# Kernel tuning notes

Hardware: AMD Instinct MI355X
Metric: run time of the kernel (lower is better)

Reference implementation:

```python
import jax, jax.numpy as jnp
import numpy as np

RES = 64      # resolution (D=H=W)
WIDTH = 32    # FNO channel width
MODES = 8     # retained Fourier modes per dim
NL = 4        # FNO layers
NU = 0.000185 # viscosity
FCH = 128     # projection hidden width
B = 4


def setup_inputs() -> dict:
    key = jax.random.key(0)
    ks = jax.random.split(key, 8)
    u = jax.random.normal(ks[0], (B, 3, RES, RES, RES), jnp.float32)
    s = 1.0 / (WIDTH * WIDTH)
    fc0_w = jax.random.normal(ks[1], (3, WIDTH), jnp.float32) * (1.0 / 3.0) ** 0.5
    fc0_b = jnp.zeros((WIDTH,), jnp.float32)
    # (layer, corner, in, out, m1, m2, m3, re/im)
    spec_w = jax.random.normal(ks[2], (NL, 4, WIDTH, WIDTH, MODES, MODES, MODES, 2), jnp.float32) * s
    w_pw = jax.random.normal(ks[3], (NL, WIDTH, WIDTH), jnp.float32) * (1.0 / WIDTH) ** 0.5
    b_pw = jnp.zeros((NL, WIDTH), jnp.float32)
    fc1_w = jax.random.normal(ks[4], (WIDTH, FCH), jnp.float32) * (1.0 / WIDTH) ** 0.5
    fc1_b = jnp.zeros((FCH,), jnp.float32)
    fc2_w = jax.random.normal(ks[5], (FCH, 6), jnp.float32) * (1.0 / FCH) ** 0.5
    fc2_b = jnp.zeros((6,), jnp.float32)
    return dict(u=u, fc0_w=fc0_w, fc0_b=fc0_b, spec_w=spec_w, w_pw=w_pw,
                b_pw=b_pw, fc1_w=fc1_w, fc1_b=fc1_b, fc2_w=fc2_w, fc2_b=fc2_b)


def _pointwise(x, w, b):
    # 1x1x1 conv: (B,C,D,H,W) x (C,O) -> (B,O,D,H,W)
    return jnp.einsum('bcdhw,co->bodhw', x, w) + b[None, :, None, None, None]


def _spectral_conv(x, wf):
    m = MODES
    Bn, C, D, H, W = x.shape
    ft = jnp.fft.rfftn(x, axes=(-3, -2, -1))           # (B,C,D,H,W//2+1) complex64
    w = wf[..., 0] + 1j * wf[..., 1]                   # (4,C,O,m,m,m)
    mul = lambda blk, ww: jnp.einsum('bixyz,ioxyz->boxyz', blk, ww)
    out = jnp.zeros((Bn, w.shape[2], D, H, W // 2 + 1), jnp.complex64)
    out = out.at[:, :, :m, :m, :m].set(mul(ft[:, :, :m, :m, :m], w[0]))
    out = out.at[:, :, -m:, :m, :m].set(mul(ft[:, :, -m:, :m, :m], w[1]))
    out = out.at[:, :, :m, -m:, :m].set(mul(ft[:, :, :m, -m:, :m], w[2]))
    out = out.at[:, :, -m:, -m:, :m].set(mul(ft[:, :, -m:, -m:, :m], w[3]))
    return jnp.fft.irfftn(out, s=(D, H, W), axes=(-3, -2, -1))


def _fno(u, fc0_w, fc0_b, spec_w, w_pw, b_pw, fc1_w, fc1_b, fc2_w, fc2_b):
    x = _pointwise(u, fc0_w, fc0_b)
    for l in range(NL):
        x1 = _spectral_conv(x, spec_w[l])
        x2 = _pointwise(x, w_pw[l], b_pw[l])
        x = x1 + x2
        if l < NL - 1:
            x = jax.nn.gelu(x)
    x = jax.nn.gelu(_pointwise(x, fc1_w, fc1_b))
    return _pointwise(x, fc2_w, fc2_b)


def _ns_hard_core(u):
    # du/dt = -(u.grad)u + nu * lap(u), periodic central differences
    dx = 2.0 * np.pi / RES
    conv = jnp.zeros_like(u)
    diff = jnp.zeros_like(u)
    for j in range(3):
        ax = 2 + j
        up = jnp.roll(u, -1, axis=ax)
        um = jnp.roll(u, 1, axis=ax)
        du = (up - um) / (2.0 * dx)          # d u_i / d x_j for all i
        conv = conv - u[:, j:j + 1] * du
        diff = diff + (up - 2.0 * u + um) / (dx * dx)
    return conv + NU * diff


def reference(u, fc0_w, fc0_b, spec_w, w_pw, b_pw, fc1_w, fc1_b, fc2_w, fc2_b):
    du_hard = _ns_hard_core(u)
    tau = _fno(u, fc0_w, fc0_b, spec_w, w_pw, b_pw, fc1_w, fc1_b, fc2_w, fc2_b)
    du_dt = du_hard + tau[:, :3] * 0.001
    return du_dt, tau
```

## Files before the change

### kernel.cpp

```cpp
#include <hip/hip_runtime.h>
#include <hip/hip_bf16.h>

#define RES 64
#define WIDTH 32
#define MODES 8
#define R3 262144
#define TWO_PI_OVER_64 0.09817477042468103f

__device__ __forceinline__ float geluf(float x) {
    float g = 1.5957691216057308f * (x + 0.044715f * x * x * x);
    return x * __builtin_amdgcn_rcpf(1.0f + __expf(-g));
}

constexpr double tcos_(double x) {
    double r = 1.0, term = 1.0;
    for (int i = 1; i <= 12; i++) { term *= -x * x / ((2.0 * i - 1.0) * (2.0 * i)); r += term; }
    return r;
}
constexpr double tsin_(double x) {
    double r = x, term = x;
    for (int i = 1; i <= 12; i++) { term *= -x * x / ((2.0 * i) * (2.0 * i + 1.0)); r += term; }
    return r;
}
struct Tw64 { float c[64]; float s[64]; };
constexpr Tw64 mkTw() {
    Tw64 t{};
    const double th = 6.283185307179586476925286766559 / 64.0;
    for (int i = 0; i < 64; i++) {
        double a = th * (i <= 32 ? i : i - 64);
        t.c[i] = (float)tcos_(a);
        t.s[i] = (float)tsin_(a);
    }
    return t;
}
constexpr Tw64 TWT = mkTw();

__global__ void k_fc0(const float* __restrict__ u, const float* __restrict__ w,
                      const float* __restrict__ bias, float* __restrict__ X) {
    __shared__ float ws[96];
    __shared__ float bs[32];
    int t = threadIdx.x;
    if (t < 96) ws[t] = w[t];
    if (t < 32) bs[t] = bias[t];
    __syncthreads();
    size_t s = (size_t)blockIdx.x * 256 + t;
    int b = (int)(s >> 18);
    size_t p = s & (R3 - 1);
    const float* ub = u + (size_t)b * 3 * R3;
    float u0 = ub[p], u1 = ub[R3 + p], u2 = ub[2 * R3 + p];
    float* xb = X + (size_t)b * 32 * R3;
    #pragma unroll
    for (int o = 0; o < 32; o++) {
        xb[(size_t)o * R3 + p] = bs[o] + u0 * ws[o] + u1 * ws[32 + o] + u2 * ws[64 + o];
    }
}

__global__ void __launch_bounds__(256, 6)
k_fwd_zy(const float* __restrict__ X, float2* __restrict__ S2) {
    int t = threadIdx.x;
    int q = t >> 6, y = t & 63;
    int bcx0 = blockIdx.x * 4;
    __shared__ float2 zt[4][8][66];
    __shared__ float2 tw[64];
    if (t < 64) { float s, c; __sincosf(TWO_PI_OVER_64 * t, &s, &c); tw[t] = make_float2(c, s); }

    const float* row = X + (size_t)(bcx0 + q) * 4096 + (size_t)y * 64;
    float re[8], im[8];
    #pragma unroll
    for (int k = 0; k < 8; k++) { re[k] = 0.f; im[k] = 0.f; }
    #pragma unroll
    for (int zb = 0; zb < 8; zb++) {
        float xa[4], xb4[4];
        *(float4*)xa  = *(const float4*)(row + zb * 4);
        *(float4*)xb4 = *(const float4*)(row + zb * 4 + 32);
        #pragma unroll
        for (int j = 0; j < 4; j++) {
            int z = zb * 4 + j;
            float sv = xa[j] + xb4[j];
            float dv = xa[j] - xb4[j];
            #pragma unroll
            for (int k = 0; k < 8; k++) {
                float v = (k & 1) ? dv : sv;
                re[k] += v * TWT.c[(k * z) & 63];
                im[k] -= v * TWT.s[(k * z) & 63];
            }
        }
    }
    #pragma unroll
    for (int k = 0; k < 8; k++) zt[q][k][y] = make_float2(re[k], im[k]);
    __syncthreads();

    int l = t & 63;
    int jy = l >> 2, kp = l & 3;
    int f = jy < 8 ? jy : 48 + jy;
    int k0 = kp * 2;
    float re0 = 0.f, im0 = 0.f, re1 = 0.f, im1 = 0.f;
    #pragma unroll 8
    for (int yy = 0; yy < 64; yy++) {
        float2 w = tw[(f * yy) & 63];
        float2 v0 = zt[q][k0][yy];
        float2 v1 = zt[q][k0 + 1][yy];
        re0 += v0.x * w.x + v0.y * w.y;
        im0 += v0.y * w.x - v0.x * w.y;
        re1 += v1.x * w.x + v1.y * w.y;
        im1 += v1.y * w.x - v1.x * w.y;
    }
    float2* dst = S2 + (size_t)(bcx0 + q) * 128 + jy * 8 + k0;
    dst[0] = make_float2(re0, im0);
    dst[1] = make_float2(re1, im1);
}

__global__ void k_fwd_x(const float2* __restrict__ S2, float2* __restrict__ S3) {
    int bc = blockIdx.x >> 3, kz = blockIdx.x & 7;
    int t = threadIdx.x;
    __shared__ float2 in[64 * 16];
    __shared__ float2 tw[64];
    if (t < 64) { float s, c; __sincosf(TWO_PI_OVER_64 * t, &s, &c); tw[t] = make_float2(c, s); }
    #pragma unroll
    for (int i = 0; i < 4; i++) {
        int e = t + 256 * i;
        in[e] = S2[((size_t)bc * 1024 + e) * 8 + kz];
    }
    __syncthreads();
    int jx = t >> 4, jy = t & 15;
    int f = jx < 8 ? jx : 48 + jx;
    float re = 0.f, im = 0.f;
    for (int x = 0; x < 64; x++) {
        float2 v = in[x * 16 + jy];
        float2 w = tw[(f * x) & 63];
        re += v.x * w.x + v.y * w.y;
        im += v.y * w.x - v.x * w.y;
    }
    S3[(size_t)bc * 2048 + (size_t)t * 8 + kz] = make_float2(re, im);
}

__global__ void k_specmul(const float2* __restrict__ S3, const float* __restrict__ spec_w,
                          float2* __restrict__ S4, int layer) {
    int mp = blockIdx.x;
    int t = threadIdx.x;
    int jxy = mp >> 2;
    int kz0 = (mp & 3) * 2;
    int jy = jxy & 15, jx = jxy >> 4;
    int corner = (jx >= 8 ? 1 : 0) + (jy >= 8 ? 2 : 0);
    int m1 = jx & 7, m2 = jy & 7;
    int mode0 = jxy * 8 + kz0;
    __shared__ float4 W4[1024];
    __shared__ float2 inb[2][128];
    const float* wbase = spec_w + (size_t)layer * 4194304 + (size_t)corner * 1048576
                       + m1 * 128 + m2 * 16 + kz0 * 2;
    #pragma unroll
    for (int j = 0; j < 8; j++) {
        int e = t + 128 * j;
        int i = e >> 5, o = e & 31;
        W4[e] = *(const float4*)(wbase + (size_t)i * 32768 + (size_t)o * 1024);
    }
    inb[0][t] = S3[(size_t)t * 2048 + mode0];
    inb[1][t] = S3[(size_t)t * 2048 + mode0 + 1];
    __syncthreads();
    int b = t >> 5, o = t & 31;
    float re0 = 0.f, im0 = 0.f, re1 = 0.f, im1 = 0.f;
    #pragma unroll 8
    for (int i = 0; i < 32; i++) {
        float2 a0 = inb[0][b * 32 + i];
        float2 a1 = inb[1][b * 32 + i];
        float4 w = W4[i * 32 + o];
        re0 += a0.x * w.x - a0.y * w.y;
        im0 += a0.x * w.y + a0.y * w.x;
        re1 += a1.x * w.z - a1.y * w.w;
        im1 += a1.x * w.w + a1.y * w.z;
    }
    S4[(size_t)(b * 32 + o) * 2048 + mode0]     = make_float2(re0, im0);
    S4[(size_t)(b * 32 + o) * 2048 + mode0 + 1] = make_float2(re1, im1);
}

__global__ void k_inv_x(const float2* __restrict__ S4, float2* __restrict__ S5) {
    int bo = blockIdx.x >> 3, kz = blockIdx.x & 7;
    int t = threadIdx.x;
    __shared__ float2 in[256];
    __shared__ float2 tw[64];
    if (t < 64) { float s, c; __sincosf(TWO_PI_OVER_64 * t, &s, &c); tw[t] = make_float2(c, s); }
    in[t] = S4[(size_t)bo * 2048 + (size_t)t * 8 + kz];
    __syncthreads();
    int x = t & 63, g = t >> 6;
    #pragma unroll
    for (int m = 0; m < 4; m++) {
        int jy = g + 4 * m;
        float re = 0.f, im = 0.f;
        #pragma unroll
        for (int jx = 0; jx < 16; jx++) {
            int f = jx < 8 ? jx : 48 + jx;
            float2 v = in[jx * 16 + jy];
            float2 w = tw[(f * x) & 63];
            re += v.x * w.x - v.y * w.y;
            im += v.x * w.y + v.y * w.x;
        }
        S5[((size_t)bo * 64 + x) * 128 + jy * 8 + kz] = make_float2(re, im);
    }
}

__global__ void __launch_bounds__(256, 3)
k_inv_yz_pw(const float2* __restrict__ S5, const float* __restrict__ w_pw,
            const float* __restrict__ b_pw, float* __restrict__ X,
            int layer, int do_gelu) {
    int blk = blockIdx.x;
    int yg = blk & 3, x = (blk >> 2) & 63, b = blk >> 8;
    int t = threadIdx.x;
    __shared__ float2 s5s[32 * 132];
    __shared__ float2 st[256];
    __shared__ float xt[2048];
    __shared__ float2 tw[64];
    if (t < 64) { float s, c; __sincosf(TWO_PI_OVER_64 * t, &s, &c); tw[t] = make_float2(c, s); }
    #pragma unroll
    for (int i = 0; i < 8; i++) {
        int f4 = t + 256 * i;
        int o = f4 >> 6, j4 = f4 & 63;
        float4 v = ((const float4*)(S5 + ((size_t)(b * 32 + o) * 64 + x) * 128))[j4];
        *(float4*)(&s5s[o * 132 + j4 * 2]) = v;
    }
    __syncthreads();
    int z = t & 63, og = t >> 6;
    int og8 = og * 8;
    int og8u = __builtin_amdgcn_readfirstlane(og8);
    const float* wl = w_pw + layer * 1024 + og8u;
    const float* bl = b_pw + layer * 32 + og8u;
    float bt0 = bl[0], bt1 = bl[1], bt2 = bl[2], bt3 = bl[3];
    float bt4 = bl[4], bt5 = bl[5], bt6 = bl[6], bt7 = bl[7];
    float2 tz1 = tw[z];
    float2 tz2 = tw[(2 * z) & 63];
    float2 tz3 = tw[(3 * z) & 63];
    float2 tz4 = tw[(4 * z) & 63];
    float2 tz5 = tw[(5 * z) & 63];
    float2 tz6 = tw[(6 * z) & 63];
    float2 tz7 = tw[(7 * z) & 63];
    const float inv_n = 1.0f / 262144.0f;
    for (int yi = 0; yi < 16; yi++) {
        int y = yg * 16 + yi;
        {
            int o = t >> 3, k = t & 7;
            float re = 0.f, im = 0.f;
            #pragma unroll
            for (int jy = 0; jy < 16; jy++) {
                int f = jy < 8 ? jy : 48 + jy;
                float2 v = s5s[o * 132 + jy * 8 + k];
                float2 w = tw[(f * y) & 63];
                re += v.x * w.x - v.y * w.y;
                im += v.x * w.y + v.y * w.x;
            }
            st[t] = make_float2(re, im);
        }
        size_t base = (size_t)b * 8388608 + (size_t)(x * 64 + y) * 64;
        #pragma unroll
        for (int i = 0; i < 8; i++) {
            int e = t + 256 * i;
            int c = e >> 6, zz = e & 63;
            xt[e] = X[base + (size_t)c * R3 + zz];
        }
        __syncthreads();
#define INVZ_S(o) (st[(o) * 8 + 0].x \
        + 2.f * (st[(o) * 8 + 1].x * tz1.x - st[(o) * 8 + 1].y * tz1.y) \
        + 2.f * (st[(o) * 8 + 2].x * tz2.x - st[(o) * 8 + 2].y * tz2.y) \
        + 2.f * (st[(o) * 8 + 3].x * tz3.x - st[(o) * 8 + 3].y * tz3.y) \
        + 2.f * (st[(o) * 8 + 4].x * tz4.x - st[(o) * 8 + 4].y * tz4.y) \
        + 2.f * (st[(o) * 8 + 5].x * tz5.x - st[(o) * 8 + 5].y * tz5.y) \
        + 2.f * (st[(o) * 8 + 6].x * tz6.x - st[(o) * 8 + 6].y * tz6.y) \
        + 2.f * (st[(o) * 8 + 7].x * tz7.x - st[(o) * 8 + 7].y * tz7.y))
        float acc0 = bt0 + INVZ_S(og8 + 0) * inv_n;
        float acc1 = bt1 + INVZ_S(og8 + 1) * inv_n;
        float acc2 = bt2 + INVZ_S(og8 + 2) * inv_n;
        float acc3 = bt3 + INVZ_S(og8 + 3) * inv_n;
        float acc4 = bt4 + INVZ_S(og8 + 4) * inv_n;
        float acc5 = bt5 + INVZ_S(og8 + 5) * inv_n;
        float acc6 = bt6 + INVZ_S(og8 + 6) * inv_n;
        float acc7 = bt7 + INVZ_S(og8 + 7) * inv_n;
#undef INVZ_S
        #pragma unroll 4
        for (int c = 0; c < 32; c++) {
            float xc = xt[c * 64 + z];
            const float* wr = wl + c * 32;
            float w0 = wr[0], w1 = wr[1], w2 = wr[2], w3 = wr[3];
            float w4 = wr[4], w5 = wr[5], w6 = wr[6], w7 = wr[7];
            acc0 += xc * w0; acc1 += xc * w1; acc2 += xc * w2; acc3 += xc * w3;
            acc4 += xc * w4; acc5 += xc * w5; acc6 += xc * w6; acc7 += xc * w7;
        }
        __syncthreads();
        float r;
        r = do_gelu ? geluf(acc0) : acc0; X[base + (size_t)(og8 + 0) * R3 + z] = r;
        r = do_gelu ? geluf(acc1) : acc1; X[base + (size_t)(og8 + 1) * R3 + z] = r;
        r = do_gelu ? geluf(acc2) : acc2; X[base + (size_t)(og8 + 2) * R3 + z] = r;
        r = do_gelu ? geluf(acc3) : acc3; X[base + (size_t)(og8 + 3) * R3 + z] = r;
        r = do_gelu ? geluf(acc4) : acc4; X[base + (size_t)(og8 + 4) * R3 + z] = r;
        r = do_gelu ? geluf(acc5) : acc5; X[base + (size_t)(og8 + 5) * R3 + z] = r;
        r = do_gelu ? geluf(acc6) : acc6; X[base + (size_t)(og8 + 6) * R3 + z] = r;
        r = do_gelu ? geluf(acc7) : acc7; X[base + (size_t)(og8 + 7) * R3 + z] = r;
    }
}

typedef short bf16x8_t __attribute__((ext_vector_type(8)));
typedef float f32x4_t __attribute__((ext_vector_type(4)));

__device__ __forceinline__ float dpp_add16(float v) {
    int i;
    i = __builtin_amdgcn_update_dpp(0, __builtin_bit_cast(int, v), 0xB1, 0xF, 0xF, true);
    v += __builtin_bit_cast(float, i);
    i = __builtin_amdgcn_update_dpp(0, __builtin_bit_cast(int, v), 0x4E, 0xF, 0xF, true);
    v += __builtin_bit_cast(float, i);
    i = __builtin_amdgcn_update_dpp(0, __builtin_bit_cast(int, v), 0x141, 0xF, 0xF, true);
    v += __builtin_bit_cast(float, i);
    i = __builtin_amdgcn_update_dpp(0, __builtin_bit_cast(int, v), 0x140, 0xF, 0xF, true);
    v += __builtin_bit_cast(float, i);
    return v;
}

__global__ void __launch_bounds__(256, 2)
k_head(const float* __restrict__ X, const float* __restrict__ w1,
       const float* __restrict__ b1, const float* __restrict__ w2,
       const float* __restrict__ b2, float* __restrict__ tau_out) {
    int t = threadIdx.x;
    int lane = t & 63;
    int wv = t >> 6;
    int m = lane & 15;
    int g = lane >> 4;
    size_t sblock = (size_t)blockIdx.x * 256;
    int b = (int)(sblock >> 18);
    size_t pblock = sblock & (R3 - 1);
    const float* xb = X + (size_t)b * 8388608 + pblock;

    bf16x8_t Bhi[8], Blo[8];
    #pragma unroll
    for (int tt = 0; tt < 8; tt++) {
        #pragma unroll
        for (int j = 0; j < 8; j++) {
            float w = w1[(g * 8 + j) * 128 + tt * 16 + m];
            unsigned bits = __builtin_bit_cast(unsigned, w);
            float hf = __builtin_bit_cast(float, bits & 0xFFFF0000u);
            float lof = w - hf;
            unsigned lb = __builtin_bit_cast(unsigned, lof);
            Bhi[tt][j] = (short)(bits >> 16);
            Blo[tt][j] = (short)(lb >> 16);
        }
    }
    float w2r[8][6];
    #pragma unroll
    for (int tt = 0; tt < 8; tt++)
        #pragma unroll
        for (int o = 0; o < 6; o++) w2r[tt][o] = w2[(tt * 16 + m) * 6 + o];
    float b1r[8];
    #pragma unroll
    for (int tt = 0; tt < 8; tt++) b1r[tt] = b1[tt * 16 + m];
    float b2m = b2[m < 6 ? m : 0];

    for (int it = 0; it < 4; it++) {
        int s16 = wv * 64 + it * 16;
        bf16x8_t Ahi, Alo;
        #pragma unroll
        for (int j = 0; j < 8; j++) {
            float xv = xb[(size_t)(g * 8 + j) * R3 + s16 + m];
            unsigned bits = __builtin_bit_cast(unsigned, xv);
            float hf = __builtin_bit_cast(float, bits & 0xFFFF0000u);
            float lof = xv - hf;
            unsigned lb = __builtin_bit_cast(unsigned, lof);
            Ahi[j] = (short)(bits >> 16);
            Alo[j] = (short)(lb >> 16);
        }
        float p0[6] = {0.f, 0.f, 0.f, 0.f, 0.f, 0.f};
        float p1[6] = {0.f, 0.f, 0.f, 0.f, 0.f, 0.f};
        float p2[6] = {0.f, 0.f, 0.f, 0.f, 0.f, 0.f};
        float p3[6] = {0.f, 0.f, 0.f, 0.f, 0.f, 0.f};
        #pragma unroll
        for (int tt = 0; tt < 8; tt++) {
            f32x4_t d = {0.f, 0.f, 0.f, 0.f};
            d = __builtin_amdgcn_mfma_f32_16x16x32_bf16(Ahi, Bhi[tt], d, 0, 0, 0);
            d = __builtin_amdgcn_mfma_f32_16x16x32_bf16(Ahi, Blo[tt], d, 0, 0, 0);
            d = __builtin_amdgcn_mfma_f32_16x16x32_bf16(Alo, Bhi[tt], d, 0, 0, 0);
            float a0 = geluf(d[0] + b1r[tt]);
            float a1 = geluf(d[1] + b1r[tt]);
            float a2 = geluf(d[2] + b1r[tt]);
            float a3 = geluf(d[3] + b1r[tt]);
            #pragma unroll
            for (int o = 0; o < 6; o++) {
                float w = w2r[tt][o];
                p0[o] += a0 * w; p1[o] += a1 * w; p2[o] += a2 * w; p3[o] += a3 * w;
            }
        }
        float q0 = 0.f, q1 = 0.f, q2 = 0.f, q3 = 0.f;
        #pragma unroll
        for (int o = 0; o < 6; o++) {
            float r0 = dpp_add16(p0[o]);
            float r1 = dpp_add16(p1[o]);
            float r2 = dpp_add16(p2[o]);
            float r3 = dpp_add16(p3[o]);
            q0 = (m == o) ? r0 : q0;
            q1 = (m == o) ? r1 : q1;
            q2 = (m == o) ? r2 : q2;
            q3 = (m == o) ? r3 : q3;
        }
        if (m < 6) {
            float4 vv = make_float4(q0 + b2m, q1 + b2m, q2 + b2m, q3 + b2m);
            *(float4*)(tau_out + (size_t)b * 6 * R3 + (size_t)m * R3 + pblock + s16 + g * 4) = vv;
        }
    }
}

__global__ void k_hard(const float* __restrict__ u, const float* __restrict__ tau,
                       float* __restrict__ out0) {
    size_t s = (size_t)blockIdx.x * 256 + threadIdx.x;
    int bi = (int)(s >> 18);
    int b = bi / 3, i = bi % 3;
    size_t p = s & (R3 - 1);
    int x = (int)(p >> 12), y = ((int)p >> 6) & 63, z = (int)p & 63;
    const float dx = TWO_PI_OVER_64;
    const float inv2dx = 1.0f / (2.0f * dx);
    const float invdx2 = 1.0f / (dx * dx);
    const float* ub = u + (size_t)b * 3 * R3;
    const float* ui = ub + (size_t)i * R3;
    int xp = (x + 1) & 63, xm = (x + 63) & 63;
    int yp = (y + 1) & 63, ym = (y + 63) & 63;
    int zp = (z + 1) & 63, zm = (z + 63) & 63;
    float c0 = ui[p];
    float upx = ui[((size_t)xp << 12) | (y << 6) | z], umx = ui[((size_t)xm << 12) | (y << 6) | z];
    float upy = ui[((size_t)x << 12) | (yp << 6) | z], umy = ui[((size_t)x << 12) | (ym << 6) | z];
    float upz = ui[((size_t)x << 12) | (y << 6) | zp], umz = ui[((size_t)x << 12) | (y << 6) | zm];
    float u0c = ub[p], u1c = ub[R3 + p], u2c = ub[2 * R3 + p];
    float conv = -(u0c * (upx - umx) + u1c * (upy - umy) + u2c * (upz - umz)) * inv2dx;
    float diff = (upx + umx + upy + umy + upz + umz - 6.0f * c0) * invdx2;
    float tauv = tau[(size_t)b * 6 * R3 + (size_t)i * R3 + p];
    out0[s] = conv + 0.000185f * diff + 0.001f * tauv;
}

extern "C" void kernel_launch(void* const* d_in, const int* in_sizes, int n_in,
                              void* d_out, int out_size, void* d_ws, size_t ws_size,
                              hipStream_t stream) {
    const float* u      = (const float*)d_in[0];
    const float* fc0_w  = (const float*)d_in[1];
    const float* fc0_b  = (const float*)d_in[2];
    const float* spec_w = (const float*)d_in[3];
    const float* w_pw   = (const float*)d_in[4];
    const float* b_pw   = (const float*)d_in[5];
    const float* fc1_w  = (const float*)d_in[6];
    const float* fc1_b  = (const float*)d_in[7];
    const float* fc2_w  = (const float*)d_in[8];
    const float* fc2_b  = (const float*)d_in[9];
    float* out = (float*)d_out;

    float* X = (float*)d_ws;

    float2* S2 = (float2*)(out);
    float2* S3 = (float2*)(out + 2097152);
    float2* S4 = (float2*)(out + 2621440);
    float2* S5 = (float2*)(out + 3145728);

    k_fc0<<<4096, 256, 0, stream>>>(u, fc0_w, fc0_b, X);

    for (int l = 0; l < 4; l++) {
        k_fwd_zy<<<2048, 256, 0, stream>>>(X, S2);
        k_fwd_x<<<1024, 256, 0, stream>>>(S2, S3);
        k_specmul<<<1024, 128, 0, stream>>>(S3, spec_w, S4, l);
        k_inv_x<<<1024, 256, 0, stream>>>(S4, S5);
        k_inv_yz_pw<<<1024, 256, 0, stream>>>(S5, w_pw, b_pw, X, l, (l < 3) ? 1 : 0);
    }

    float* tau_out = out + (size_t)4 * 3 * R3;
    k_head<<<4096, 256, 0, stream>>>(X, fc1_w, fc1_b, fc2_w, fc2_b, tau_out);
    k_hard<<<12288, 256, 0, stream>>>(u, tau_out, out);
}
```

Baseline: 1.123 ms.

## Keep spectral coefficients in registers and prefetch next X row in inverse yz kernel

The inverse y/z transform plus pointwise kernel no longer stages the per-x spectral slab in shared memory. Each thread now loads its 16 coefficients straight into registers, and the next y-row of X is prefetched into registers while the current row is being computed. Dropping the large shared buffer frees LDS, and launch bounds go from 3 to 4 blocks per CU to raise occupancy. The trade-off is more register pressure, which could cause spills under the tighter bound, and uncoalesced strided global loads for the coefficients.

```diff
diff --git a/kernel.cpp b/kernel.cpp
--- a/kernel.cpp
+++ b/kernel.cpp
@@ -198,26 +198,24 @@
     }
 }
 
-__global__ void __launch_bounds__(256, 3)
+__global__ void __launch_bounds__(256, 4)
 k_inv_yz_pw(const float2* __restrict__ S5, const float* __restrict__ w_pw,
             const float* __restrict__ b_pw, float* __restrict__ X,
             int layer, int do_gelu) {
     int blk = blockIdx.x;
     int yg = blk & 3, x = (blk >> 2) & 63, b = blk >> 8;
     int t = threadIdx.x;
-    __shared__ float2 s5s[32 * 132];
     __shared__ float2 st[256];
     __shared__ float xt[2048];
     __shared__ float2 tw[64];
     if (t < 64) { float s, c; __sincosf(TWO_PI_OVER_64 * t, &s, &c); tw[t] = make_float2(c, s); }
-    #pragma unroll
-    for (int i = 0; i < 8; i++) {
-        int f4 = t + 256 * i;
-        int o = f4 >> 6, j4 = f4 & 63;
-        float4 v = ((const float4*)(S5 + ((size_t)(b * 32 + o) * 64 + x) * 128))[j4];
-        *(float4*)(&s5s[o * 132 + j4 * 2]) = v;
-    }
-    __syncthreads();
+
+    int oA = t >> 3, kA = t & 7;
+    float2 sr[16];
+    const float2* s5p = S5 + ((size_t)(b * 32 + oA) * 64 + x) * 128 + kA;
+    #pragma unroll
+    for (int jy = 0; jy < 16; jy++) sr[jy] = s5p[jy * 8];
+
     int z = t & 63, og = t >> 6;
     int og8 = og * 8;
     int og8u = __builtin_amdgcn_readfirstlane(og8);
@@ -225,37 +223,52 @@
     const float* bl = b_pw + layer * 32 + og8u;
     float bt0 = bl[0], bt1 = bl[1], bt2 = bl[2], bt3 = bl[3];
     float bt4 = bl[4], bt5 = bl[5], bt6 = bl[6], bt7 = bl[7];
-    float2 tz1 = tw[z];
-    float2 tz2 = tw[(2 * z) & 63];
-    float2 tz3 = tw[(3 * z) & 63];
-    float2 tz4 = tw[(4 * z) & 63];
-    float2 tz5 = tw[(5 * z) & 63];
-    float2 tz6 = tw[(6 * z) & 63];
-    float2 tz7 = tw[(7 * z) & 63];
+    float2 tz1, tz2, tz3, tz4, tz5, tz6, tz7;
+    {
+        __syncthreads();
+        tz1 = tw[z];
+        tz2 = tw[(2 * z) & 63];
+        tz3 = tw[(3 * z) & 63];
+        tz4 = tw[(4 * z) & 63];
+        tz5 = tw[(5 * z) & 63];
+        tz6 = tw[(6 * z) & 63];
+        tz7 = tw[(7 * z) & 63];
+    }
     const float inv_n = 1.0f / 262144.0f;
+
+    size_t base0 = (size_t)b * 8388608 + (size_t)(x * 64 + yg * 16) * 64;
+    float xr[8];
+    #pragma unroll
+    for (int i = 0; i < 8; i++) {
+        int e = t + 256 * i;
+        xr[i] = X[base0 + (size_t)(e >> 6) * R3 + (e & 63)];
+    }
+
     for (int yi = 0; yi < 16; yi++) {
         int y = yg * 16 + yi;
+        size_t base = base0 + (size_t)yi * 64;
+        #pragma unroll
+        for (int i = 0; i < 8; i++) xt[t + 256 * i] = xr[i];
         {
-            int o = t >> 3, k = t & 7;
             float re = 0.f, im = 0.f;
             #pragma unroll
             for (int jy = 0; jy < 16; jy++) {
                 int f = jy < 8 ? jy : 48 + jy;
-                float2 v = s5s[o * 132 + jy * 8 + k];
                 float2 w = tw[(f * y) & 63];
-                re += v.x * w.x - v.y * w.y;
-                im += v.x * w.y + v.y * w.x;
+                re += sr[jy].x * w.x - sr[jy].y * w.y;
+                im += sr[jy].x * w.y + sr[jy].y * w.x;
             }
             st[t] = make_float2(re, im);
         }
-        size_t base = (size_t)b * 8388608 + (size_t)(x * 64 + y) * 64;
-        #pragma unroll
-        for (int i = 0; i < 8; i++) {
-            int e = t + 256 * i;
-            int c = e >> 6, zz = e & 63;
-            xt[e] = X[base + (size_t)c * R3 + zz];
-        }
         __syncthreads();
+        if (yi < 15) {
+            size_t nbase = base + 64;
+            #pragma unroll
+            for (int i = 0; i < 8; i++) {
+                int e = t + 256 * i;
+                xr[i] = X[nbase + (size_t)(e >> 6) * R3 + (e & 63)];
+            }
+        }
 #define INVZ_S(o) (st[(o) * 8 + 0].x \
         + 2.f * (st[(o) * 8 + 1].x * tz1.x - st[(o) * 8 + 1].y * tz1.y) \
         + 2.f * (st[(o) * 8 + 2].x * tz2.x - st[(o) * 8 + 2].y * tz2.y) \
```

New measurement: 1.427 ms. 1.27x slower.
